# Optimization experiments

Measured on AMD Instinct MI355X. Metric: run time of the kernel, lower is better.

The kernel has to match this reference:

```python
import jax, jax.numpy as jnp
import numpy as np

V, E = 100000, 128
B, Q, D = 512, 32, 256
K_NUM, SIGMA, EXACT_SIGMA = 21, 0.1, 0.001
EPS = 1e-8


def _kernel_params():
    # faithful to source (including the sigma/exact_sigma swap at the call site)
    l_mu = [1.0]
    bin_size = 2.0 / (K_NUM - 1)
    l_mu.append(1 - bin_size / 2)
    for j in range(1, K_NUM - 1):
        l_mu.append(l_mu[j] - bin_size)
    mus = sorted(l_mu)
    # kernel_sigmas(n, sigma=exact_sigma, exact_sigma=sigma) due to swapped call
    sig_list = [SIGMA] + [EXACT_SIGMA] * (K_NUM - 1)
    sigmas = sorted(sig_list)[::-1]
    return (jnp.asarray(mus, dtype=jnp.float32),
            jnp.asarray(sigmas, dtype=jnp.float32))

MUS, SIGMAS = _kernel_params()


def setup_inputs() -> dict:
    key = jax.random.key(0)
    ks = jax.random.split(key, 11)
    emb = jax.random.normal(ks[0], (V, E), dtype=jnp.float32)
    emb = emb.at[0].set(0.0)  # padding_idx=0
    w1 = jax.random.normal(ks[1], (K_NUM, 10), dtype=jnp.float32) / np.sqrt(K_NUM)
    b1 = jax.random.normal(ks[2], (10,), dtype=jnp.float32) * 0.01
    w2 = jax.random.normal(ks[3], (10, 5), dtype=jnp.float32) / np.sqrt(10)
    b2 = jax.random.normal(ks[4], (5,), dtype=jnp.float32) * 0.01
    w3 = jax.random.normal(ks[5], (5, 1), dtype=jnp.float32) / np.sqrt(5)
    b3 = jax.random.normal(ks[6], (1,), dtype=jnp.float32) * 0.01
    query1 = jax.random.randint(ks[7], (B, Q), 0, V, dtype=jnp.int64 if jax.config.jax_enable_x64 else jnp.int32)
    doc1 = jax.random.randint(ks[8], (B, D), 0, V, dtype=query1.dtype)
    query2 = jax.random.randint(ks[9], (B, Q), 0, V, dtype=query1.dtype)
    doc2 = jax.random.randint(ks[10], (B, D), 0, V, dtype=query1.dtype)
    return {"emb": emb, "w1": w1, "b1": b1, "w2": w2, "b2": b2,
            "w3": w3, "b3": b3, "query1": query1, "doc1": doc1,
            "query2": query2, "doc2": doc2}


def _l2norm(x):
    n = jnp.linalg.norm(x, axis=-1, keepdims=True)
    return x / jnp.maximum(n, EPS)


def _predict(emb, w1, b1, w2, b2, w3, b3, q_idx, d_idx):
    q_idx = jnp.clip(q_idx, 0, V - 1)
    d_idx = jnp.clip(d_idx, 0, V - 1)
    qn = _l2norm(emb[q_idx])            # [B,Q,E]
    dn = _l2norm(emb[d_idx])            # [B,D,E]
    mm = jnp.einsum('bqe,bde->bqd', qn, dn)  # cosine matching matrix [B,Q,D]
    # soft-histogram Gaussian kernel pooling: [B,Q,D,K]
    phi = jnp.exp(-0.5 * (mm[..., None] - MUS) ** 2 / SIGMAS ** 2)
    k_out = jnp.log1p(phi.sum(axis=2)).sum(axis=1)  # [B,K]
    x = jax.nn.relu(k_out) @ w1 + b1
    x = jax.nn.relu(x) @ w2 + b2
    x = jax.nn.relu(x) @ w3 + b3
    return x  # [B,1]


def reference(emb, w1, b1, w2, b2, w3, b3, query1, doc1, query2, doc2):
    logits_1 = _predict(emb, w1, b1, w2, b2, w3, b3, query1, doc1)
    logits_2 = _predict(emb, w1, b1, w2, b2, w3, b3, query2, doc2)
    return jax.nn.sigmoid(logits_1 - logits_2)
```

## Files before the change

kernel.cpp:

```cpp
#include <hip/hip_runtime.h>
#include <math.h>

#define V_SIZE 100000
#define E_DIM  128
#define B_SIZE 512
#define Q_LEN  32
#define D_LEN  256
#define K_NUM  21


typedef _Float16 half8_t  __attribute__((ext_vector_type(8)));
typedef float    float4_t __attribute__((ext_vector_type(4)));

__global__ __launch_bounds__(256, 4) void knrm_main(
    const float* __restrict__ emb,
    const int* __restrict__ q1, const int* __restrict__ d1,
    const int* __restrict__ q2, const int* __restrict__ d2,
    const float* __restrict__ w1, const float* __restrict__ b1,
    const float* __restrict__ w2, const float* __restrict__ b2,
    const float* __restrict__ w3, const float* __restrict__ b3,
    float* __restrict__ logits)
{
    const int b    = blockIdx.x;
    const int pair = blockIdx.y;
    const int t    = threadIdx.x;
    const int* __restrict__ qidx = pair ? q2 : q1;
    const int* __restrict__ didx = pair ? d2 : d1;

    __shared__ half8_t AfH[2][4][64];
    __shared__ half8_t AfL[2][4][64];
    __shared__ float rnq[Q_LEN];
    __shared__ float phis[Q_LEN][22];
    __shared__ float ko[K_NUM];

    const int lane = t & 63;
    const int w    = t >> 6;
    const int quad = lane >> 4;
    const int l15  = lane & 15;

    for (int i = t; i < Q_LEN * 22; i += 256) ((float*)phis)[i] = 0.f;

    {
        const int qr = t >> 3;
        const int qc = t & 7;
        int qi = qidx[b * Q_LEN + qr];
        qi = min(max(qi, 0), V_SIZE - 1);
        const float4* src = (const float4*)(emb + (size_t)qi * E_DIM) + qc * 4;
        float4 v0 = src[0], v1 = src[1], v2 = src[2], v3 = src[3];
        float fv[16] = {v0.x,v0.y,v0.z,v0.w, v1.x,v1.y,v1.z,v1.w,
                        v2.x,v2.y,v2.z,v2.w, v3.x,v3.y,v3.z,v3.w};
        float ss = 0.f;
        half8_t h0, h1, l0, l1;
        #pragma unroll
        for (int j = 0; j < 8; ++j) {
            ss = fmaf(fv[j], fv[j], ss);
            _Float16 h = (_Float16)fv[j];
            h0[j] = h; l0[j] = (_Float16)(fv[j] - (float)h);
        }
        #pragma unroll
        for (int j = 0; j < 8; ++j) {
            ss = fmaf(fv[8 + j], fv[8 + j], ss);
            _Float16 h = (_Float16)fv[8 + j];
            h1[j] = h; l1[j] = (_Float16)(fv[8 + j] - (float)h);
        }
        const int qt  = qr >> 4;
        const int lr  = qr & 15;
        const int s   = qc >> 1;
        const int qd0 = (qc & 1) * 2;
        AfH[qt][s][qd0 * 16 + lr]       = h0;
        AfH[qt][s][(qd0 + 1) * 16 + lr] = h1;
        AfL[qt][s][qd0 * 16 + lr]       = l0;
        AfL[qt][s][(qd0 + 1) * 16 + lr] = l1;
        ss += __shfl_xor(ss, 1, 8);
        ss += __shfl_xor(ss, 2, 8);
        ss += __shfl_xor(ss, 4, 8);
        if (qc == 0) rnq[qr] = 1.0f / fmaxf(sqrtf(ss), 1e-8f);
    }
    __syncthreads();

    float rnqv[8];
    #pragma unroll
    for (int i = 0; i < 8; ++i) rnqv[i] = rnq[(i >> 2) * 16 + quad * 4 + (i & 3)];

    const float cc0 = -0.5f / (0.1f * 0.1f);
    const float ccs = -0.5f / (0.001f * 0.001f);
    float breg[8] = {0.f,0.f,0.f,0.f,0.f,0.f,0.f,0.f};

    int dix[4];
    #pragma unroll
    for (int c = 0; c < 4; ++c) {
        int di = didx[b * D_LEN + w * 64 + c * 16 + l15];
        dix[c] = min(max(di, 0), V_SIZE - 1);
    }

    half8_t bh[4], bl[4];
    float rnd;

    auto convert = [&](const float4* v) {
        float ss = 0.f;
        #pragma unroll
        for (int s = 0; s < 4; ++s) {
            float f[8] = {v[2*s].x, v[2*s].y, v[2*s].z, v[2*s].w,
                          v[2*s+1].x, v[2*s+1].y, v[2*s+1].z, v[2*s+1].w};
            half8_t h, l;
            #pragma unroll
            for (int j = 0; j < 8; ++j) {
                ss = fmaf(f[j], f[j], ss);
                _Float16 hh = (_Float16)f[j];
                h[j] = hh; l[j] = (_Float16)(f[j] - (float)hh);
            }
            bh[s] = h; bl[s] = l;
        }
        ss += __shfl_xor(ss, 16);
        ss += __shfl_xor(ss, 32);
        rnd = 1.0f / fmaxf(sqrtf(ss), 1e-8f);
    };

    {
        const float4* dr = (const float4*)(emb + (size_t)dix[0] * E_DIM) + quad * 2;
        float4 cur[8];
        #pragma unroll
        for (int s = 0; s < 4; ++s) { cur[2*s] = dr[s*8]; cur[2*s+1] = dr[s*8+1]; }
        convert(cur);
    }

    #pragma unroll
    for (int c = 0; c < 4; ++c) {
        float4 nx[8];
        if (c < 3) {
            const float4* dr = (const float4*)(emb + (size_t)dix[c+1] * E_DIM) + quad * 2;
            #pragma unroll
            for (int s = 0; s < 4; ++s) { nx[2*s] = dr[s*8]; nx[2*s+1] = dr[s*8+1]; }
        }

        float4_t acc0 = {0.f,0.f,0.f,0.f}, acc1 = {0.f,0.f,0.f,0.f};
        #pragma unroll
        for (int s = 0; s < 4; ++s) {
            half8_t a0h = AfH[0][s][lane], a0l = AfL[0][s][lane];
            half8_t a1h = AfH[1][s][lane], a1l = AfL[1][s][lane];
            acc0 = __builtin_amdgcn_mfma_f32_16x16x32_f16(a0h, bh[s], acc0, 0, 0, 0);
            acc1 = __builtin_amdgcn_mfma_f32_16x16x32_f16(a1h, bh[s], acc1, 0, 0, 0);
            acc0 = __builtin_amdgcn_mfma_f32_16x16x32_f16(a0l, bh[s], acc0, 0, 0, 0);
            acc1 = __builtin_amdgcn_mfma_f32_16x16x32_f16(a1l, bh[s], acc1, 0, 0, 0);
            acc0 = __builtin_amdgcn_mfma_f32_16x16x32_f16(a0h, bl[s], acc0, 0, 0, 0);
            acc1 = __builtin_amdgcn_mfma_f32_16x16x32_f16(a1h, bl[s], acc1, 0, 0, 0);
        }

        #pragma unroll
        for (int qt = 0; qt < 2; ++qt) {
            const float4_t acc = qt ? acc1 : acc0;
            #pragma unroll
            for (int r = 0; r < 4; ++r) {
                const float mm = acc[r] * rnqv[qt*4 + r] * rnd;
                const float x0 = mm + 0.95f;
                breg[qt*4 + r] += __expf(x0 * x0 * cc0);
                float g = rintf((mm + 0.85f) * 10.f);
                g = fminf(fmaxf(g, 0.f), 18.f);
                float mu = fmaf(g, 0.1f, -0.85f);
                int ks = (int)g + 1;
                if (mm > 0.975f) { mu = 1.0f; ks = 20; }
                const float xs = mm - mu;
                const float es = __expf(xs * xs * ccs);
                if (es > 0.f) atomicAdd(&phis[qt*16 + quad*4 + r][ks], es);
            }
        }

        if (c < 3) convert(nx);
    }

    #pragma unroll
    for (int i = 0; i < 8; ++i) {
        float v = breg[i];
        v += __shfl_xor(v, 1, 16);
        v += __shfl_xor(v, 2, 16);
        v += __shfl_xor(v, 4, 16);
        v += __shfl_xor(v, 8, 16);
        if (l15 == 0) atomicAdd(&phis[(i >> 2) * 16 + quad * 4 + (i & 3)][0], v);
    }
    __syncthreads();

    for (int p = t; p < K_NUM * Q_LEN; p += 256) {
        const int q = p & 31;
        const int k = p >> 5;
        float l = log1pf(phis[q][k]);
        l += __shfl_xor(l, 1, 32);
        l += __shfl_xor(l, 2, 32);
        l += __shfl_xor(l, 4, 32);
        l += __shfl_xor(l, 8, 32);
        l += __shfl_xor(l, 16, 32);
        if (q == 0) ko[k] = l;
    }
    __syncthreads();

    if (t == 0) {
        float x1v[10];
        #pragma unroll
        for (int i = 0; i < 10; ++i) {
            float s = b1[i];
            for (int k = 0; k < K_NUM; ++k) {
                float v = ko[k] > 0.f ? ko[k] : 0.f;
                s = fmaf(v, w1[k * 10 + i], s);
            }
            x1v[i] = s;
        }
        float x2v[5];
        #pragma unroll
        for (int i = 0; i < 5; ++i) {
            float s = b2[i];
            #pragma unroll
            for (int k = 0; k < 10; ++k) {
                float v = x1v[k] > 0.f ? x1v[k] : 0.f;
                s = fmaf(v, w2[k * 5 + i], s);
            }
            x2v[i] = s;
        }
        float s3 = b3[0];
        #pragma unroll
        for (int k = 0; k < 5; ++k) {
            float v = x2v[k] > 0.f ? x2v[k] : 0.f;
            s3 = fmaf(v, w3[k], s3);
        }
        logits[pair * B_SIZE + b] = s3;
    }
}

__global__ void knrm_final(const float* __restrict__ logits, float* __restrict__ out)
{
    const int b = blockIdx.x * blockDim.x + threadIdx.x;
    if (b < B_SIZE) {
        const float dl = logits[b] - logits[B_SIZE + b];
        out[b] = 1.0f / (1.0f + __expf(-dl));
    }
}

extern "C" void kernel_launch(void* const* d_in, const int* in_sizes, int n_in,
                              void* d_out, int out_size, void* d_ws, size_t ws_size,
                              hipStream_t stream)
{
    const float* emb = (const float*)d_in[0];
    const float* w1  = (const float*)d_in[1];
    const float* b1  = (const float*)d_in[2];
    const float* w2  = (const float*)d_in[3];
    const float* b2  = (const float*)d_in[4];
    const float* w3  = (const float*)d_in[5];
    const float* b3  = (const float*)d_in[6];
    const int*   q1  = (const int*)d_in[7];
    const int*   d1  = (const int*)d_in[8];
    const int*   q2  = (const int*)d_in[9];
    const int*   d2  = (const int*)d_in[10];

    float* logits = (float*)d_ws;
    float* out    = (float*)d_out;

    dim3 grid(B_SIZE, 2);
    knrm_main<<<grid, 256, 0, stream>>>(emb, q1, d1, q2, d2,
                                        w1, b1, w2, b2, w3, b3, logits);
    knrm_final<<<(B_SIZE + 255) / 256, 256, 0, stream>>>(logits, out);
}
```

Baseline: 124.7 us.

## Split doc dimension across two blocks and move pooling/MLP into reduce kernel

Each batch/pair is now handled by two blocks that each cover half of the document tokens, giving twice as many blocks. Every wave issues both of its doc-row loads up front, before the query staging, and computes two 16-column tiles with interleaved MFMAs instead of running a four-step software pipeline. Partial per-query kernel sums go to a global workspace. A new reduce kernel combines the halves, applies log1p, sums over queries, runs the MLP and the sigmoid, which replaces the old final kernel. This adds parallelism and latency hiding, at the cost of a global round-trip for the partial histograms and duplicated query loading in both split blocks.

```diff
diff --git a/kernel.cpp b/kernel.cpp
--- a/kernel.cpp
+++ b/kernel.cpp
@@ -1,29 +1,28 @@
 #include <hip/hip_runtime.h>
 #include <math.h>
 
-#define V_SIZE 100000
-#define E_DIM  128
-#define B_SIZE 512
-#define Q_LEN  32
-#define D_LEN  256
-#define K_NUM  21
+#define V_SIZE  100000
+#define E_DIM   128
+#define B_SIZE  512
+#define Q_LEN   32
+#define D_LEN   256
+#define K_NUM   21
+#define PHI_STR 24
 
 
 typedef _Float16 half8_t  __attribute__((ext_vector_type(8)));
 typedef float    float4_t __attribute__((ext_vector_type(4)));
 
-__global__ __launch_bounds__(256, 4) void knrm_main(
+__global__ __launch_bounds__(256, 4) void knrm_gemm(
     const float* __restrict__ emb,
     const int* __restrict__ q1, const int* __restrict__ d1,
     const int* __restrict__ q2, const int* __restrict__ d2,
-    const float* __restrict__ w1, const float* __restrict__ b1,
-    const float* __restrict__ w2, const float* __restrict__ b2,
-    const float* __restrict__ w3, const float* __restrict__ b3,
-    float* __restrict__ logits)
+    float* __restrict__ phis_g)
 {
-    const int b    = blockIdx.x;
-    const int pair = blockIdx.y;
-    const int t    = threadIdx.x;
+    const int b     = blockIdx.x;
+    const int pair  = blockIdx.y;
+    const int split = blockIdx.z;
+    const int t     = threadIdx.x;
     const int* __restrict__ qidx = pair ? q2 : q1;
     const int* __restrict__ didx = pair ? d2 : d1;
 
@@ -31,7 +30,6 @@
     __shared__ half8_t AfL[2][4][64];
     __shared__ float rnq[Q_LEN];
     __shared__ float phis[Q_LEN][22];
-    __shared__ float ko[K_NUM];
 
     const int lane = t & 63;
     const int w    = t >> 6;
@@ -39,6 +37,23 @@
     const int l15  = lane & 15;
 
     for (int i = t; i < Q_LEN * 22; i += 256) ((float*)phis)[i] = 0.f;
+
+    const int dbase = split * 128 + w * 32;
+    int di0 = didx[b * D_LEN + dbase + l15];
+    int di1 = didx[b * D_LEN + dbase + 16 + l15];
+    di0 = min(max(di0, 0), V_SIZE - 1);
+    di1 = min(max(di1, 0), V_SIZE - 1);
+    const float4* dr0 = (const float4*)(emb + (size_t)di0 * E_DIM) + quad * 2;
+    const float4* dr1 = (const float4*)(emb + (size_t)di1 * E_DIM) + quad * 2;
+    float4 raw0[8], raw1[8];
+    #pragma unroll
+    for (int s = 0; s < 4; ++s) {
+        raw0[2*s]   = dr0[s*8];
+        raw0[2*s+1] = dr0[s*8+1];
+        raw1[2*s]   = dr1[s*8];
+        raw1[2*s+1] = dr1[s*8+1];
+    }
+    __builtin_amdgcn_sched_barrier(0);
 
     {
         const int qr = t >> 3;
@@ -82,26 +97,14 @@
     #pragma unroll
     for (int i = 0; i < 8; ++i) rnqv[i] = rnq[(i >> 2) * 16 + quad * 4 + (i & 3)];
 
-    const float cc0 = -0.5f / (0.1f * 0.1f);
-    const float ccs = -0.5f / (0.001f * 0.001f);
-    float breg[8] = {0.f,0.f,0.f,0.f,0.f,0.f,0.f,0.f};
-
-    int dix[4];
-    #pragma unroll
-    for (int c = 0; c < 4; ++c) {
-        int di = didx[b * D_LEN + w * 64 + c * 16 + l15];
-        dix[c] = min(max(di, 0), V_SIZE - 1);
-    }
-
-    half8_t bh[4], bl[4];
-    float rnd;
-
-    auto convert = [&](const float4* v) {
+    half8_t bh0[4], bl0[4], bh1[4], bl1[4];
+    float rnd0, rnd1;
+    {
         float ss = 0.f;
         #pragma unroll
         for (int s = 0; s < 4; ++s) {
-            float f[8] = {v[2*s].x, v[2*s].y, v[2*s].z, v[2*s].w,
-                          v[2*s+1].x, v[2*s+1].y, v[2*s+1].z, v[2*s+1].w};
+            float f[8] = {raw0[2*s].x, raw0[2*s].y, raw0[2*s].z, raw0[2*s].w,
+                          raw0[2*s+1].x, raw0[2*s+1].y, raw0[2*s+1].z, raw0[2*s+1].w};
             half8_t h, l;
             #pragma unroll
             for (int j = 0; j < 8; ++j) {
@@ -109,49 +112,64 @@
                 _Float16 hh = (_Float16)f[j];
                 h[j] = hh; l[j] = (_Float16)(f[j] - (float)hh);
             }
-            bh[s] = h; bl[s] = l;
+            bh0[s] = h; bl0[s] = l;
         }
         ss += __shfl_xor(ss, 16);
         ss += __shfl_xor(ss, 32);
-        rnd = 1.0f / fmaxf(sqrtf(ss), 1e-8f);
-    };
-
+        rnd0 = 1.0f / fmaxf(sqrtf(ss), 1e-8f);
+    }
     {
-        const float4* dr = (const float4*)(emb + (size_t)dix[0] * E_DIM) + quad * 2;
-        float4 cur[8];
-        #pragma unroll
-        for (int s = 0; s < 4; ++s) { cur[2*s] = dr[s*8]; cur[2*s+1] = dr[s*8+1]; }
-        convert(cur);
-    }
-
-    #pragma unroll
-    for (int c = 0; c < 4; ++c) {
-        float4 nx[8];
-        if (c < 3) {
-            const float4* dr = (const float4*)(emb + (size_t)dix[c+1] * E_DIM) + quad * 2;
-            #pragma unroll
-            for (int s = 0; s < 4; ++s) { nx[2*s] = dr[s*8]; nx[2*s+1] = dr[s*8+1]; }
-        }
-
-        float4_t acc0 = {0.f,0.f,0.f,0.f}, acc1 = {0.f,0.f,0.f,0.f};
+        float ss = 0.f;
         #pragma unroll
         for (int s = 0; s < 4; ++s) {
-            half8_t a0h = AfH[0][s][lane], a0l = AfL[0][s][lane];
-            half8_t a1h = AfH[1][s][lane], a1l = AfL[1][s][lane];
-            acc0 = __builtin_amdgcn_mfma_f32_16x16x32_f16(a0h, bh[s], acc0, 0, 0, 0);
-            acc1 = __builtin_amdgcn_mfma_f32_16x16x32_f16(a1h, bh[s], acc1, 0, 0, 0);
-            acc0 = __builtin_amdgcn_mfma_f32_16x16x32_f16(a0l, bh[s], acc0, 0, 0, 0);
-            acc1 = __builtin_amdgcn_mfma_f32_16x16x32_f16(a1l, bh[s], acc1, 0, 0, 0);
-            acc0 = __builtin_amdgcn_mfma_f32_16x16x32_f16(a0h, bl[s], acc0, 0, 0, 0);
-            acc1 = __builtin_amdgcn_mfma_f32_16x16x32_f16(a1h, bl[s], acc1, 0, 0, 0);
-        }
-
-        #pragma unroll
-        for (int qt = 0; qt < 2; ++qt) {
-            const float4_t acc = qt ? acc1 : acc0;
+            float f[8] = {raw1[2*s].x, raw1[2*s].y, raw1[2*s].z, raw1[2*s].w,
+                          raw1[2*s+1].x, raw1[2*s+1].y, raw1[2*s+1].z, raw1[2*s+1].w};
+            half8_t h, l;
+            #pragma unroll
+            for (int j = 0; j < 8; ++j) {
+                ss = fmaf(f[j], f[j], ss);
+                _Float16 hh = (_Float16)f[j];
+                h[j] = hh; l[j] = (_Float16)(f[j] - (float)hh);
+            }
+            bh1[s] = h; bl1[s] = l;
+        }
+        ss += __shfl_xor(ss, 16);
+        ss += __shfl_xor(ss, 32);
+        rnd1 = 1.0f / fmaxf(sqrtf(ss), 1e-8f);
+    }
+
+    float4_t acc00 = {0,0,0,0}, acc01 = {0,0,0,0};
+    float4_t acc10 = {0,0,0,0}, acc11 = {0,0,0,0};
+    #pragma unroll
+    for (int s = 0; s < 4; ++s) {
+        half8_t a0h = AfH[0][s][lane], a0l = AfL[0][s][lane];
+        half8_t a1h = AfH[1][s][lane], a1l = AfL[1][s][lane];
+        acc00 = __builtin_amdgcn_mfma_f32_16x16x32_f16(a0h, bh0[s], acc00, 0, 0, 0);
+        acc01 = __builtin_amdgcn_mfma_f32_16x16x32_f16(a0h, bh1[s], acc01, 0, 0, 0);
+        acc10 = __builtin_amdgcn_mfma_f32_16x16x32_f16(a1h, bh0[s], acc10, 0, 0, 0);
+        acc11 = __builtin_amdgcn_mfma_f32_16x16x32_f16(a1h, bh1[s], acc11, 0, 0, 0);
+        acc00 = __builtin_amdgcn_mfma_f32_16x16x32_f16(a0l, bh0[s], acc00, 0, 0, 0);
+        acc01 = __builtin_amdgcn_mfma_f32_16x16x32_f16(a0l, bh1[s], acc01, 0, 0, 0);
+        acc10 = __builtin_amdgcn_mfma_f32_16x16x32_f16(a1l, bh0[s], acc10, 0, 0, 0);
+        acc11 = __builtin_amdgcn_mfma_f32_16x16x32_f16(a1l, bh1[s], acc11, 0, 0, 0);
+        acc00 = __builtin_amdgcn_mfma_f32_16x16x32_f16(a0h, bl0[s], acc00, 0, 0, 0);
+        acc01 = __builtin_amdgcn_mfma_f32_16x16x32_f16(a0h, bl1[s], acc01, 0, 0, 0);
+        acc10 = __builtin_amdgcn_mfma_f32_16x16x32_f16(a1h, bl0[s], acc10, 0, 0, 0);
+        acc11 = __builtin_amdgcn_mfma_f32_16x16x32_f16(a1h, bl1[s], acc11, 0, 0, 0);
+    }
+
+    const float cc0 = -0.5f / (0.1f * 0.1f);
+    const float ccs = -0.5f / (0.001f * 0.001f);
+    float breg[8] = {0.f,0.f,0.f,0.f,0.f,0.f,0.f,0.f};
+    #pragma unroll
+    for (int qt = 0; qt < 2; ++qt) {
+        #pragma unroll
+        for (int dt = 0; dt < 2; ++dt) {
+            const float4_t acc = qt ? (dt ? acc11 : acc10) : (dt ? acc01 : acc00);
+            const float rdv = dt ? rnd1 : rnd0;
             #pragma unroll
             for (int r = 0; r < 4; ++r) {
-                const float mm = acc[r] * rnqv[qt*4 + r] * rnd;
+                const float mm = acc[r] * rnqv[qt*4 + r] * rdv;
                 const float x0 = mm + 0.95f;
                 breg[qt*4 + r] += __expf(x0 * x0 * cc0);
                 float g = rintf((mm + 0.85f) * 10.f);
@@ -164,10 +182,7 @@
                 if (es > 0.f) atomicAdd(&phis[qt*16 + quad*4 + r][ks], es);
             }
         }
-
-        if (c < 3) convert(nx);
-    }
-
+    }
     #pragma unroll
     for (int i = 0; i < 8; ++i) {
         float v = breg[i];
@@ -179,26 +194,50 @@
     }
     __syncthreads();
 
-    for (int p = t; p < K_NUM * Q_LEN; p += 256) {
-        const int q = p & 31;
-        const int k = p >> 5;
-        float l = log1pf(phis[q][k]);
-        l += __shfl_xor(l, 1, 32);
-        l += __shfl_xor(l, 2, 32);
-        l += __shfl_xor(l, 4, 32);
-        l += __shfl_xor(l, 8, 32);
-        l += __shfl_xor(l, 16, 32);
-        if (q == 0) ko[k] = l;
-    }
-    __syncthreads();
-
-    if (t == 0) {
+    const size_t gbase = (size_t)((split * 2 + pair) * B_SIZE + b) * Q_LEN * PHI_STR;
+    for (int i = t; i < Q_LEN * K_NUM; i += 256) {
+        const int q = i / K_NUM;
+        const int k = i - q * K_NUM;
+        phis_g[gbase + q * PHI_STR + k] = phis[q][k];
+    }
+}
+
+__global__ __launch_bounds__(64) void knrm_reduce(
+    const float* __restrict__ phis_g,
+    const float* __restrict__ w1, const float* __restrict__ b1,
+    const float* __restrict__ w2, const float* __restrict__ b2,
+    const float* __restrict__ w3, const float* __restrict__ b3,
+    float* __restrict__ out)
+{
+    const int b = blockIdx.x;
+    const int t = threadIdx.x;
+    const int p = t >> 5;
+    const int q = t & 31;
+
+    const float* g0 = phis_g + ((size_t)((0 + p) * B_SIZE + b) * Q_LEN + q) * PHI_STR;
+    const float* g1 = phis_g + ((size_t)((2 + p) * B_SIZE + b) * Q_LEN + q) * PHI_STR;
+
+    float lp[K_NUM];
+    #pragma unroll
+    for (int k = 0; k < K_NUM; ++k) lp[k] = log1pf(g0[k] + g1[k]);
+    #pragma unroll
+    for (int k = 0; k < K_NUM; ++k) {
+        lp[k] += __shfl_xor(lp[k], 1, 32);
+        lp[k] += __shfl_xor(lp[k], 2, 32);
+        lp[k] += __shfl_xor(lp[k], 4, 32);
+        lp[k] += __shfl_xor(lp[k], 8, 32);
+        lp[k] += __shfl_xor(lp[k], 16, 32);
+    }
+
+    float logit = 0.f;
+    if (q == 0) {
         float x1v[10];
         #pragma unroll
         for (int i = 0; i < 10; ++i) {
             float s = b1[i];
+            #pragma unroll
             for (int k = 0; k < K_NUM; ++k) {
-                float v = ko[k] > 0.f ? ko[k] : 0.f;
+                float v = lp[k] > 0.f ? lp[k] : 0.f;
                 s = fmaf(v, w1[k * 10 + i], s);
             }
             x1v[i] = s;
@@ -220,15 +259,11 @@
             float v = x2v[k] > 0.f ? x2v[k] : 0.f;
             s3 = fmaf(v, w3[k], s3);
         }
-        logits[pair * B_SIZE + b] = s3;
-    }
-}
-
-__global__ void knrm_final(const float* __restrict__ logits, float* __restrict__ out)
-{
-    const int b = blockIdx.x * blockDim.x + threadIdx.x;
-    if (b < B_SIZE) {
-        const float dl = logits[b] - logits[B_SIZE + b];
+        logit = s3;
+    }
+    const float l2 = __shfl(logit, 32);
+    if (t == 0) {
+        const float dl = logit - l2;
         out[b] = 1.0f / (1.0f + __expf(-dl));
     }
 }
@@ -249,11 +284,10 @@
     const int*   q2  = (const int*)d_in[9];
     const int*   d2  = (const int*)d_in[10];
 
-    float* logits = (float*)d_ws;
+    float* phis_g = (float*)d_ws;
     float* out    = (float*)d_out;
 
-    dim3 grid(B_SIZE, 2);
-    knrm_main<<<grid, 256, 0, stream>>>(emb, q1, d1, q2, d2,
-                                        w1, b1, w2, b2, w3, b3, logits);
-    knrm_final<<<(B_SIZE + 255) / 256, 256, 0, stream>>>(logits, out);
+    dim3 grid(B_SIZE, 2, 2);
+    knrm_gemm<<<grid, 256, 0, stream>>>(emb, q1, d1, q2, d2, phis_g);
+    knrm_reduce<<<B_SIZE, 64, 0, stream>>>(phis_g, w1, b1, w2, b2, w3, b3, out);
 }
```

After: 139.0 us. 11.4% more time.

## Stage doc embedding rows via async global-to-LDS loads and move MLP to final kernel

Applied to the files above, without the earlier changes.

Doc embedding rows are now copied with global_load_lds straight into a per-wave 32KB LDS staging buffer. The loop waits on vmcnt before reading the row, converts it, then issues the async load for the next row while the MFMAs run. This replaces the register-held prefetch and should lower VGPR use, but the extra LDS cuts occupancy (launch bounds go from 4 to 3) and adds explicit waits. The tiny MLP also moves out of the main kernel into the final kernel, which now reads the per-pair 21-wide kernel outputs from the workspace, and the loop is no longer unrolled.

```diff
diff --git a/kernel.cpp b/kernel.cpp
--- a/kernel.cpp
+++ b/kernel.cpp
@@ -1,24 +1,24 @@
 #include <hip/hip_runtime.h>
 #include <math.h>
 
-#define V_SIZE 100000
-#define E_DIM  128
-#define B_SIZE 512
-#define Q_LEN  32
-#define D_LEN  256
-#define K_NUM  21
+#define V_SIZE  100000
+#define E_DIM   128
+#define B_SIZE  512
+#define Q_LEN   32
+#define D_LEN   256
+#define K_NUM   21
 
 
 typedef _Float16 half8_t  __attribute__((ext_vector_type(8)));
 typedef float    float4_t __attribute__((ext_vector_type(4)));
 
-__global__ __launch_bounds__(256, 4) void knrm_main(
+#define GLOBAL_AS __attribute__((address_space(1)))
+#define LDS_AS    __attribute__((address_space(3)))
+
+__global__ __launch_bounds__(256, 3) void knrm_gemm(
     const float* __restrict__ emb,
     const int* __restrict__ q1, const int* __restrict__ d1,
     const int* __restrict__ q2, const int* __restrict__ d2,
-    const float* __restrict__ w1, const float* __restrict__ b1,
-    const float* __restrict__ w2, const float* __restrict__ b2,
-    const float* __restrict__ w3, const float* __restrict__ b3,
     float* __restrict__ logits)
 {
     const int b    = blockIdx.x;
@@ -27,6 +27,7 @@
     const int* __restrict__ qidx = pair ? q2 : q1;
     const int* __restrict__ didx = pair ? d2 : d1;
 
+    __shared__ __align__(16) unsigned char stage[4][8192];
     __shared__ half8_t AfH[2][4][64];
     __shared__ half8_t AfL[2][4][64];
     __shared__ float rnq[Q_LEN];
@@ -39,6 +40,24 @@
     const int l15  = lane & 15;
 
     for (int i = t; i < Q_LEN * 22; i += 256) ((float*)phis)[i] = 0.f;
+
+    const unsigned char* grow[4];
+    #pragma unroll
+    for (int c = 0; c < 4; ++c) {
+        int di = didx[b * D_LEN + w * 64 + c * 16 + l15];
+        di = min(max(di, 0), V_SIZE - 1);
+        grow[c] = (const unsigned char*)(emb + (size_t)di * E_DIM) + quad * 32;
+    }
+
+    #pragma unroll
+    for (int s = 0; s < 4; ++s) {
+        #pragma unroll
+        for (int h = 0; h < 2; ++h) {
+            __builtin_amdgcn_global_load_lds(
+                (const GLOBAL_AS void*)(grow[0] + s * 128 + h * 16),
+                (LDS_AS void*)(&stage[w][(s * 2 + h) * 1024]), 16, 0, 0);
+        }
+    }
 
     {
         const int qr = t >> 3;
@@ -86,22 +105,17 @@
     const float ccs = -0.5f / (0.001f * 0.001f);
     float breg[8] = {0.f,0.f,0.f,0.f,0.f,0.f,0.f,0.f};
 
-    int dix[4];
-    #pragma unroll
+    #pragma unroll 1
     for (int c = 0; c < 4; ++c) {
-        int di = didx[b * D_LEN + w * 64 + c * 16 + l15];
-        dix[c] = min(max(di, 0), V_SIZE - 1);
-    }
-
-    half8_t bh[4], bl[4];
-    float rnd;
-
-    auto convert = [&](const float4* v) {
+        asm volatile("s_waitcnt vmcnt(0)" ::: "memory");
+
+        half8_t bh[4], bl[4];
         float ss = 0.f;
         #pragma unroll
         for (int s = 0; s < 4; ++s) {
-            float f[8] = {v[2*s].x, v[2*s].y, v[2*s].z, v[2*s].w,
-                          v[2*s+1].x, v[2*s+1].y, v[2*s+1].z, v[2*s+1].w};
+            float4 v0 = *(const float4*)&stage[w][(s * 2 + 0) * 1024 + lane * 16];
+            float4 v1 = *(const float4*)&stage[w][(s * 2 + 1) * 1024 + lane * 16];
+            float f[8] = {v0.x,v0.y,v0.z,v0.w, v1.x,v1.y,v1.z,v1.w};
             half8_t h, l;
             #pragma unroll
             for (int j = 0; j < 8; ++j) {
@@ -113,27 +127,22 @@
         }
         ss += __shfl_xor(ss, 16);
         ss += __shfl_xor(ss, 32);
-        rnd = 1.0f / fmaxf(sqrtf(ss), 1e-8f);
-    };
-
-    {
-        const float4* dr = (const float4*)(emb + (size_t)dix[0] * E_DIM) + quad * 2;
-        float4 cur[8];
-        #pragma unroll
-        for (int s = 0; s < 4; ++s) { cur[2*s] = dr[s*8]; cur[2*s+1] = dr[s*8+1]; }
-        convert(cur);
-    }
-
-    #pragma unroll
-    for (int c = 0; c < 4; ++c) {
-        float4 nx[8];
+        const float rnd = 1.0f / fmaxf(sqrtf(ss), 1e-8f);
+
+        asm volatile("s_waitcnt lgkmcnt(0)" ::: "memory");
         if (c < 3) {
-            const float4* dr = (const float4*)(emb + (size_t)dix[c+1] * E_DIM) + quad * 2;
-            #pragma unroll
-            for (int s = 0; s < 4; ++s) { nx[2*s] = dr[s*8]; nx[2*s+1] = dr[s*8+1]; }
-        }
-
-        float4_t acc0 = {0.f,0.f,0.f,0.f}, acc1 = {0.f,0.f,0.f,0.f};
+            #pragma unroll
+            for (int s = 0; s < 4; ++s) {
+                #pragma unroll
+                for (int h = 0; h < 2; ++h) {
+                    __builtin_amdgcn_global_load_lds(
+                        (const GLOBAL_AS void*)(grow[c + 1] + s * 128 + h * 16),
+                        (LDS_AS void*)(&stage[w][(s * 2 + h) * 1024]), 16, 0, 0);
+                }
+            }
+        }
+
+        float4_t acc0 = {0,0,0,0}, acc1 = {0,0,0,0};
         #pragma unroll
         for (int s = 0; s < 4; ++s) {
             half8_t a0h = AfH[0][s][lane], a0l = AfL[0][s][lane];
@@ -151,9 +160,9 @@
             const float4_t acc = qt ? acc1 : acc0;
             #pragma unroll
             for (int r = 0; r < 4; ++r) {
-                const float mm = acc[r] * rnqv[qt*4 + r] * rnd;
+                const float mm = acc[r] * rnqv[qt * 4 + r] * rnd;
                 const float x0 = mm + 0.95f;
-                breg[qt*4 + r] += __expf(x0 * x0 * cc0);
+                breg[qt * 4 + r] += __expf(x0 * x0 * cc0);
                 float g = rintf((mm + 0.85f) * 10.f);
                 g = fminf(fmaxf(g, 0.f), 18.f);
                 float mu = fmaf(g, 0.1f, -0.85f);
@@ -161,11 +170,9 @@
                 if (mm > 0.975f) { mu = 1.0f; ks = 20; }
                 const float xs = mm - mu;
                 const float es = __expf(xs * xs * ccs);
-                if (es > 0.f) atomicAdd(&phis[qt*16 + quad*4 + r][ks], es);
-            }
-        }
-
-        if (c < 3) convert(nx);
+                if (es > 0.f) atomicAdd(&phis[qt * 16 + quad * 4 + r][ks], es);
+            }
+        }
     }
 
     #pragma unroll
@@ -193,10 +200,33 @@
     __syncthreads();
 
     if (t == 0) {
+    }
+    if (t < K_NUM) {
+        logits[((size_t)pair * B_SIZE + b) * K_NUM + t] = ko[t];
+    }
+}
+
+__global__ __launch_bounds__(64) void knrm_final(
+    const float* __restrict__ kout,
+    const float* __restrict__ w1, const float* __restrict__ b1,
+    const float* __restrict__ w2, const float* __restrict__ b2,
+    const float* __restrict__ w3, const float* __restrict__ b3,
+    float* __restrict__ out)
+{
+    const int b = blockIdx.x * 32 + (threadIdx.x & 31);
+    const int p = threadIdx.x >> 5;
+    if (threadIdx.x >= 32) return;
+    if (b >= B_SIZE) return;
+
+    float logit[2];
+    #pragma unroll
+    for (int pr = 0; pr < 2; ++pr) {
+        const float* ko = kout + ((size_t)pr * B_SIZE + b) * K_NUM;
         float x1v[10];
         #pragma unroll
         for (int i = 0; i < 10; ++i) {
             float s = b1[i];
+            #pragma unroll
             for (int k = 0; k < K_NUM; ++k) {
                 float v = ko[k] > 0.f ? ko[k] : 0.f;
                 s = fmaf(v, w1[k * 10 + i], s);
@@ -220,17 +250,10 @@
             float v = x2v[k] > 0.f ? x2v[k] : 0.f;
             s3 = fmaf(v, w3[k], s3);
         }
-        logits[pair * B_SIZE + b] = s3;
-    }
-}
-
-__global__ void knrm_final(const float* __restrict__ logits, float* __restrict__ out)
-{
-    const int b = blockIdx.x * blockDim.x + threadIdx.x;
-    if (b < B_SIZE) {
-        const float dl = logits[b] - logits[B_SIZE + b];
-        out[b] = 1.0f / (1.0f + __expf(-dl));
-    }
+        logit[pr] = s3;
+    }
+    const float dl = logit[0] - logit[1];
+    out[b] = 1.0f / (1.0f + __expf(-dl));
 }
 
 extern "C" void kernel_launch(void* const* d_in, const int* in_sizes, int n_in,
@@ -249,11 +272,10 @@
     const int*   q2  = (const int*)d_in[9];
     const int*   d2  = (const int*)d_in[10];
 
-    float* logits = (float*)d_ws;
-    float* out    = (float*)d_out;
+    float* kout = (float*)d_ws;
+    float* out  = (float*)d_out;
 
     dim3 grid(B_SIZE, 2);
-    knrm_main<<<grid, 256, 0, stream>>>(emb, q1, d1, q2, d2,
-                                        w1, b1, w2, b2, w3, b3, logits);
-    knrm_final<<<(B_SIZE + 255) / 256, 256, 0, stream>>>(logits, out);
+    knrm_gemm<<<grid, 256, 0, stream>>>(emb, q1, d1, q2, d2, kout);
+    knrm_final<<<(B_SIZE + 31) / 32, 64, 0, stream>>>(kout, w1, b1, w2, b2, w3, b3, out);
 }
```

Measured after the change: 136.1 us. 1.09x slower.
